# Kernel optimization log

Hardware: AMD Instinct MI355X
Metric: run time of the kernel (lower is better)

## Reference

```python
import jax, jax.numpy as jnp
import numpy as np

K = 16        # neighbors
M = 4         # repeat count
EPS = 1e-5    # BatchNorm eps (torch default)


def setup_inputs() -> dict:
    key = jax.random.key(0)
    k1, k2, k3, k4 = jax.random.split(key, 4)
    B, N, C, Fe = 8, 8192, 64, 32  # Fe = int(channels * dim_expand)
    return {
        "xyz": jax.random.normal(k1, (B, N, 3), dtype=jnp.float32),
        "feat": jax.random.normal(k2, (B, C, N), dtype=jnp.float32),
        "bn_gamma": jnp.ones((C,), jnp.float32),
        "bn_beta": jnp.zeros((C,), jnp.float32),
        "Wg": jax.random.normal(k3, (Fe, C + 3), jnp.float32) * 0.1,   # g_func weight [out, in]
        "Wh": jax.random.normal(k4, (C, M * Fe), jnp.float32) * 0.1,   # h_func weight [out, in]
    }


def reference(xyz, feat, bn_gamma, bn_beta, Wg, Wh):
    # xyz: [B, N, 3], feat: [B, C, N]
    # --- bn0: training-mode BatchNorm1d over channel dim (stats over B, N) ---
    mean = feat.mean(axis=(0, 2), keepdims=True)
    var = feat.var(axis=(0, 2), keepdims=True)
    fbn = bn_gamma[None, :, None] * (feat - mean) * jax.lax.rsqrt(var + EPS) + bn_beta[None, :, None]

    # --- g_func on concat(feat_bn, xyz^T) -> feat0 [B, N, Fe] ---
    cat = jnp.concatenate([fbn, jnp.transpose(xyz, (0, 2, 1))], axis=1)  # [B, C+3, N]
    feat0 = jnp.einsum('bcn,ec->bne', cat, Wg)                           # [B, N, Fe]

    # --- bknn: pairwise squared distances, top-k of -dist (computed once) ---
    xx = jnp.sum(xyz * xyz, axis=-1)                                     # [B, N]
    dist = xx[:, :, None] - 2.0 * jnp.einsum('bnd,bmd->bnm', xyz, xyz) + xx[:, None, :]
    _, idx = jax.lax.top_k(-dist, K)                                     # [B, N, K] int32

    # --- gather neighbor features, max-pool over K ---
    group = jax.vmap(lambda f, i: f[i])(feat0, idx)                      # [B, N, K, Fe]
    gmax = group.max(axis=2)                                             # [B, N, Fe]
    rel = gmax - feat0                                                   # [B, N, Fe]

    # Original loop reuses cached idx and feat0 every iteration, so all M
    # concatenated blocks are identical -> tile along the feature dim.
    rel_rep = jnp.concatenate([rel] * M, axis=-1)                        # [B, N, M*Fe]

    # --- h_func -> output [B, C, N] ---
    out = jnp.einsum('bnf,cf->bcn', rel_rep, Wh)
    return out
```

## Files before the change

kernel.cpp:

```cpp
#include <hip/hip_runtime.h>
#include <math.h>

#define BB 8
#define NN 8192
#define CC 64
#define FE 32
#define KN 16
#define CP3 67
#define QPW 4
#define WPB 4
#define CAPQ 64
#define YB 32
#define ZB 32
#define NCELL (YB * ZB)

__device__ double g_part[BB * CC * 2];
__device__ float g_feat0[BB * NN * FE];
__device__ int   g_idx[BB * NN * KN];
__device__ float4 g_sorted[BB * NN];
__device__ int    g_sorig[BB * NN];
__device__ unsigned g_binoff[BB * (NCELL + 1)];

__device__ __forceinline__ int cbin(float v) {
    int bi = (int)((v + 4.5f) * (32.0f / 9.0f));
    if (bi < 0) bi = 0;
    if (bi > 31) bi = 31;
    return bi;
}
__device__ __forceinline__ float frz_xx(float x, float y, float z) {
    return __fmaf_rn(z, z, __fmaf_rn(y, y, __fmul_rn(x, x)));
}

__global__ __launch_bounds__(256) void k_bnstats(const float* __restrict__ feat) {
    int bc = blockIdx.x;
    const float* p = feat + (size_t)bc * NN;
    int tid = threadIdx.x;
    double s = 0.0, s2 = 0.0;
    for (int n = tid; n < NN; n += 256) {
        double v = (double)p[n];
        s += v; s2 += v * v;
    }
    __shared__ double sh[256], sh2[256];
    sh[tid] = s; sh2[tid] = s2;
    __syncthreads();
    for (int off = 128; off > 0; off >>= 1) {
        if (tid < off) { sh[tid] += sh[tid + off]; sh2[tid] += sh2[tid + off]; }
        __syncthreads();
    }
    if (tid == 0) {
        g_part[bc * 2]     = sh[0];
        g_part[bc * 2 + 1] = sh2[0];
    }
}

__global__ __launch_bounds__(1024) void k_zbin(const float* __restrict__ xyz) {
    __shared__ unsigned hist[NCELL];
    __shared__ unsigned scan[NCELL];
    __shared__ unsigned boff[NCELL + 1];
    int b = blockIdx.x;
    int tid = threadIdx.x;
    hist[tid] = 0;
    __syncthreads();
    const float* bx = xyz + (size_t)b * NN * 3;
    for (int n = tid; n < NN; n += 1024) {
        float y = bx[n * 3 + 1], z = bx[n * 3 + 2];
        atomicAdd(&hist[cbin(y) * ZB + cbin(z)], 1u);
    }
    __syncthreads();
    scan[tid] = hist[tid];
    __syncthreads();
    for (int off = 1; off < NCELL; off <<= 1) {
        unsigned add = (tid >= off) ? scan[tid - off] : 0u;
        __syncthreads();
        scan[tid] += add;
        __syncthreads();
    }
    if (tid == 0) boff[0] = 0;
    boff[tid + 1] = scan[tid];
    __syncthreads();
    hist[tid] = 0;
    g_binoff[b * (NCELL + 1) + tid + 1] = boff[tid + 1];
    if (tid == 0) g_binoff[b * (NCELL + 1)] = 0;
    __syncthreads();
    for (int n = tid; n < NN; n += 1024) {
        const float* p = bx + (size_t)n * 3;
        float x = p[0], y = p[1], z = p[2];
        int cell = cbin(y) * ZB + cbin(z);
        unsigned pos = boff[cell] + atomicAdd(&hist[cell], 1u);
        g_sorted[(size_t)b * NN + pos] = make_float4(x, y, z, frz_xx(x, y, z));
        g_sorig[(size_t)b * NN + pos] = n;
    }
}

__global__ __launch_bounds__(256) void k_feat0(const float* __restrict__ feat,
        const float* __restrict__ xyz, const float* __restrict__ Wg,
        const float* __restrict__ gamma, const float* __restrict__ beta) {
    __shared__ float scs[CC], shs[CC];
    __shared__ float wgs[CP3 * FE];
    __shared__ float bias0[FE];
    int tid = threadIdx.x;
    if (tid < CC) {
        double s = 0.0, s2 = 0.0;
        for (int bb2 = 0; bb2 < BB; ++bb2) {
            s  += g_part[((bb2 << 6) + tid) * 2];
            s2 += g_part[((bb2 << 6) + tid) * 2 + 1];
        }
        double inv = 1.0 / (double)(BB * NN);
        double mean = s * inv;
        double var = s2 * inv - mean * mean;
        float sc = gamma[tid] * (float)(1.0 / sqrt(var + (double)1e-5f));
        scs[tid] = sc;
        shs[tid] = beta[tid] - sc * (float)mean;
    }
    __syncthreads();
    for (int i = tid; i < CP3 * FE; i += 256) {
        int c = i >> 5, e = i & 31;
        float w = Wg[e * CP3 + c];
        if (c < CC) w *= scs[c];
        wgs[c * FE + e] = w;
    }
    if (tid < FE) {
        float sacc = 0.f;
        for (int c = 0; c < CC; ++c) sacc = fmaf(Wg[tid * CP3 + c], shs[c], sacc);
        bias0[tid] = sacc;
    }
    __syncthreads();
    int b = blockIdx.x >> 5;
    int n = ((blockIdx.x & 31) << 8) + tid;
    const float* pz = xyz + ((size_t)(b * NN + n)) * 3;
    float x = pz[0], y = pz[1], z = pz[2];

    float acc[FE];
    #pragma unroll
    for (int e = 0; e < FE; ++e) acc[e] = bias0[e];
    const float* fp = feat + (size_t)b * CC * NN + n;
    for (int c = 0; c < CC; ++c) {
        float v = fp[(size_t)c * NN];
        const float4* w4 = (const float4*)(wgs + c * FE);
        #pragma unroll
        for (int e0 = 0; e0 < 8; ++e0) {
            float4 w = w4[e0];
            acc[e0 * 4 + 0] = fmaf(w.x, v, acc[e0 * 4 + 0]);
            acc[e0 * 4 + 1] = fmaf(w.y, v, acc[e0 * 4 + 1]);
            acc[e0 * 4 + 2] = fmaf(w.z, v, acc[e0 * 4 + 2]);
            acc[e0 * 4 + 3] = fmaf(w.w, v, acc[e0 * 4 + 3]);
        }
    }
    #pragma unroll
    for (int d = 0; d < 3; ++d) {
        float v = (d == 0) ? x : ((d == 1) ? y : z);
        const float4* w4 = (const float4*)(wgs + (CC + d) * FE);
        #pragma unroll
        for (int e0 = 0; e0 < 8; ++e0) {
            float4 w = w4[e0];
            acc[e0 * 4 + 0] = fmaf(w.x, v, acc[e0 * 4 + 0]);
            acc[e0 * 4 + 1] = fmaf(w.y, v, acc[e0 * 4 + 1]);
            acc[e0 * 4 + 2] = fmaf(w.z, v, acc[e0 * 4 + 2]);
            acc[e0 * 4 + 3] = fmaf(w.w, v, acc[e0 * 4 + 3]);
        }
    }
    float4* outp = (float4*)(g_feat0 + ((size_t)(b * NN + n)) * FE);
    #pragma unroll
    for (int e0 = 0; e0 < 8; ++e0)
        outp[e0] = make_float4(acc[e0 * 4 + 0], acc[e0 * 4 + 1], acc[e0 * 4 + 2], acc[e0 * 4 + 3]);
}

__global__ __launch_bounds__(256) void k_knn() {
    __shared__ unsigned long long qbuf[WPB * CAPQ];
    int tid = threadIdx.x;
    int lane = tid & 63;
    int w = tid >> 6;
    int wid = blockIdx.x * WPB + w;
    int b = wid >> 11;
    int g = wid & 2047;
    const float4* S = g_sorted + (size_t)b * NN;
    const int* SO = g_sorig + (size_t)b * NN;
    const unsigned* BO = g_binoff + b * (NCELL + 1);
    unsigned long long lt = (1ull << lane) - 1ull;
    unsigned long long* pb = qbuf + w * CAPQ;

    #pragma unroll 1
    for (int i = 0; i < QPW; ++i) {
        int qrank = g + (i << 11);
        float4 qv = S[qrank];
        float qx = qv.x, qy = qv.y, qz = qv.z, qxx = qv.w;
        int qorig = SO[qrank];
        float tt = 0.053f * __expf(qxx * (1.0f / 3.0f));
        float t0 = tt > 3.f ? 3.f : tt;
        float tlo = 0.f, thi = 0.f;
        unsigned cnt = 0;

        for (int attempt = 0; attempt < 40; ++attempt) {
            cnt = 0;
            float tpe = t0 + 1e-3f;
            float R = __fsqrt_rn(tpe) + 1e-3f;
            int ylo = cbin(qy - R), yhi = cbin(qy + R);

            int yb = ylo, p = 0, hi = 0;
            {
                float rowlo = 0.28125f * (float)yb - 4.5f;
                float dy = fmaxf(0.f, fmaxf(rowlo - qy, qy - (rowlo + 0.28125f)));
                float rz2 = tpe - dy * dy;
                if (rz2 > 0.f) {
                    float Rz = __fsqrt_rn(rz2) + 1e-3f;
                    int zl = cbin(qz - Rz), zh = cbin(qz + Rz);
                    p = (int)BO[yb * ZB + zl]; hi = (int)BO[yb * ZB + zh + 1];
                }
            }
            while (p >= hi && yb < yhi) {
                ++yb;
                float rowlo = 0.28125f * (float)yb - 4.5f;
                float dy = fmaxf(0.f, fmaxf(rowlo - qy, qy - (rowlo + 0.28125f)));
                float rz2 = tpe - dy * dy;
                if (rz2 > 0.f) {
                    float Rz = __fsqrt_rn(rz2) + 1e-3f;
                    int zl = cbin(qz - Rz), zh = cbin(qz + Rz);
                    p = (int)BO[yb * ZB + zl]; hi = (int)BO[yb * ZB + zh + 1];
                } else { p = 0; hi = 0; }
            }
            bool have = p < hi;
            int jc0 = 0, jc1 = 0; bool in0 = false, in1 = false;
            float4 c0, c1;
            if (have) {
                int base = p + 2 * lane;
                jc0 = base < hi ? base : hi - 1;
                jc1 = base + 1 < hi ? base + 1 : hi - 1;
                c0 = S[jc0]; c1 = S[jc1];
                in0 = base < hi; in1 = base + 1 < hi;
            }
            while (have) {
                int yb2 = yb, p2 = p + 128, hi2 = hi;
                while (p2 >= hi2 && yb2 < yhi) {
                    ++yb2;
                    float rowlo = 0.28125f * (float)yb2 - 4.5f;
                    float dy = fmaxf(0.f, fmaxf(rowlo - qy, qy - (rowlo + 0.28125f)));
                    float rz2 = tpe - dy * dy;
                    if (rz2 > 0.f) {
                        float Rz = __fsqrt_rn(rz2) + 1e-3f;
                        int zl = cbin(qz - Rz), zh = cbin(qz + Rz);
                        p2 = (int)BO[yb2 * ZB + zl]; hi2 = (int)BO[yb2 * ZB + zh + 1];
                    } else { p2 = 0; hi2 = 0; }
                }
                bool have2 = p2 < hi2;
                int jn0 = jc0, jn1 = jc1; bool inn0 = false, inn1 = false;
                float4 n0 = c0, n1 = c1;
                if (have2) {
                    int base = p2 + 2 * lane;
                    jn0 = base < hi2 ? base : hi2 - 1;
                    jn1 = base + 1 < hi2 ? base + 1 : hi2 - 1;
                    n0 = S[jn0]; n1 = S[jn1];
                    inn0 = base < hi2; inn1 = base + 1 < hi2;
                }
                float dot0 = __fmaf_rn(qz, c0.z, __fmaf_rn(qy, c0.y, __fmul_rn(qx, c0.x)));
                float dist0 = __fadd_rn(__fmaf_rn(-2.f, dot0, qxx), c0.w);
                float dot1 = __fmaf_rn(qz, c1.z, __fmaf_rn(qy, c1.y, __fmul_rn(qx, c1.x)));
                float dist1 = __fadd_rn(__fmaf_rn(-2.f, dot1, qxx), c1.w);
                bool pr0 = (dist0 <= t0) && in0;
                bool pr1 = (dist1 <= t0) && in1;
                unsigned long long m0 = __ballot(pr0);
                unsigned long long m1 = __ballot(pr1);
                if (m0 | m1) {
                    unsigned n0c = (unsigned)__popcll(m0);
                    unsigned pos0 = cnt + (unsigned)__popcll(m0 & lt);
                    unsigned pos1 = cnt + n0c + (unsigned)__popcll(m1 & lt);
                    if (pr0 && pos0 < CAPQ) {
                        int corig = SO[jc0];
                        int db = __float_as_int(dist0);
                        unsigned key = (unsigned)db ^ (unsigned)((db >> 31) | 0x80000000);
                        pb[pos0] = ((unsigned long long)key << 32) | (unsigned)corig;
                    }
                    if (pr1 && pos1 < CAPQ) {
                        int corig = SO[jc1];
                        int db = __float_as_int(dist1);
                        unsigned key = (unsigned)db ^ (unsigned)((db >> 31) | 0x80000000);
                        pb[pos1] = ((unsigned long long)key << 32) | (unsigned)corig;
                    }
                    cnt += n0c + (unsigned)__popcll(m1);
                }
                yb = yb2; p = p2; hi = hi2; have = have2;
                jc0 = jn0; jc1 = jn1; c0 = n0; c1 = n1; in0 = inn0; in1 = inn1;
            }
            if (cnt < KN) {
                tlo = t0;
                t0 = (thi > 0.f) ? __fsqrt_rn(tlo * thi) : t0 * 2.0f;
            } else if (cnt > CAPQ) {
                thi = t0;
                t0 = (tlo > 0.f) ? __fsqrt_rn(tlo * thi) : t0 * 0.5f;
            } else break;
        }

        unsigned tot = cnt > CAPQ ? CAPQ : cnt;
        unsigned long long e0 = ((unsigned)lane < tot) ? pb[lane] : ~0ull;
        unsigned rank0 = 0;
        for (unsigned jx = 0; jx < tot; ++jx) {
            unsigned long long v = pb[jx];
            rank0 += (v < e0) ? 1u : 0u;
        }
        if (((unsigned)lane < tot) && rank0 < KN)
            g_idx[(b * NN + qorig) * KN + rank0] = (int)(e0 & 0xffffffffull);
    }
}

__global__ __launch_bounds__(256) void k_out(const float* __restrict__ Wh,
        float* __restrict__ out) {
    __shared__ float whs[CC * FE];
    int tid = threadIdx.x;
    for (int i = tid; i < CC * FE; i += 256) {
        int c = i >> 5, e = i & 31;
        float s = 0.f;
        #pragma unroll
        for (int m = 0; m < 4; ++m) s += Wh[c * 128 + m * 32 + e];
        whs[i] = s;
    }
    __syncthreads();
    int b = blockIdx.x >> 5;
    int n = ((blockIdx.x & 31) << 8) + tid;
    const int* ip = g_idx + (size_t)(b * NN + n) * KN;
    const float4* f0 = (const float4*)(g_feat0 + (size_t)b * NN * FE);
    float gmax[FE];
    #pragma unroll
    for (int e = 0; e < FE; ++e) gmax[e] = -__builtin_inff();
    for (int k = 0; k < KN; ++k) {
        int id = ip[k] & (NN - 1);
        const float4* row = f0 + (size_t)id * 8;
        #pragma unroll
        for (int e0 = 0; e0 < 8; ++e0) {
            float4 v = row[e0];
            gmax[e0 * 4 + 0] = fmaxf(gmax[e0 * 4 + 0], v.x);
            gmax[e0 * 4 + 1] = fmaxf(gmax[e0 * 4 + 1], v.y);
            gmax[e0 * 4 + 2] = fmaxf(gmax[e0 * 4 + 2], v.z);
            gmax[e0 * 4 + 3] = fmaxf(gmax[e0 * 4 + 3], v.w);
        }
    }
    const float4* selfr = f0 + (size_t)n * 8;
    float rel[FE];
    #pragma unroll
    for (int e0 = 0; e0 < 8; ++e0) {
        float4 v = selfr[e0];
        rel[e0 * 4 + 0] = gmax[e0 * 4 + 0] - v.x;
        rel[e0 * 4 + 1] = gmax[e0 * 4 + 1] - v.y;
        rel[e0 * 4 + 2] = gmax[e0 * 4 + 2] - v.z;
        rel[e0 * 4 + 3] = gmax[e0 * 4 + 3] - v.w;
    }
    float* op = out + (size_t)b * CC * NN + n;
    for (int c = 0; c < CC; ++c) {
        const float4* w4 = (const float4*)(whs + c * FE);
        float s = 0.f;
        #pragma unroll
        for (int e0 = 0; e0 < 8; ++e0) {
            float4 w = w4[e0];
            s = fmaf(w.x, rel[e0 * 4 + 0], s);
            s = fmaf(w.y, rel[e0 * 4 + 1], s);
            s = fmaf(w.z, rel[e0 * 4 + 2], s);
            s = fmaf(w.w, rel[e0 * 4 + 3], s);
        }
        op[(size_t)c * NN] = s;
    }
}

extern "C" void kernel_launch(void* const* d_in, const int* in_sizes, int n_in,
                              void* d_out, int out_size, void* d_ws, size_t ws_size,
                              hipStream_t stream) {
    const float* xyz   = (const float*)d_in[0];
    const float* feat  = (const float*)d_in[1];
    const float* gamma = (const float*)d_in[2];
    const float* beta  = (const float*)d_in[3];
    const float* Wg    = (const float*)d_in[4];
    const float* Wh    = (const float*)d_in[5];
    float* out = (float*)d_out;
    (void)d_ws; (void)ws_size;

    hipLaunchKernelGGL(k_bnstats, dim3(512),  dim3(256),  0, stream, feat);
    hipLaunchKernelGGL(k_zbin,    dim3(8),    dim3(1024), 0, stream, xyz);
    hipLaunchKernelGGL(k_feat0,   dim3(256),  dim3(256),  0, stream, feat, xyz, Wg, gamma, beta);
    hipLaunchKernelGGL(k_knn,     dim3(4096), dim3(256),  0, stream);
    hipLaunchKernelGGL(k_out,     dim3(256),  dim3(256),  0, stream, Wh, out);
}
```

Before: 201.0 us.

## Split per-point work across multiple threads in feat0 and output kernels

k_feat0 now gives each point to two threads, each computing 16 of the 32 features, and launches twice as many blocks. k_out gives each point to four threads: each gathers 4 of the 16 neighbors, the partial maxima are combined through shared memory, and each thread then computes 16 of the 64 output channels. This raises parallelism and occupancy in two kernels that previously launched only 256 blocks on a large GPU. The cost is a shared-memory reduction, a block barrier, and less coalesced feat loads and output stores, since adjacent threads now share a point.

```diff
diff --git a/kernel.cpp b/kernel.cpp
--- a/kernel.cpp
+++ b/kernel.cpp
@@ -125,20 +125,22 @@
         bias0[tid] = sacc;
     }
     __syncthreads();
-    int b = blockIdx.x >> 5;
-    int n = ((blockIdx.x & 31) << 8) + tid;
+    int pid = blockIdx.x * 128 + (tid >> 1);
+    int half = tid & 1;
+    int b = pid >> 13;
+    int n = pid & (NN - 1);
     const float* pz = xyz + ((size_t)(b * NN + n)) * 3;
     float x = pz[0], y = pz[1], z = pz[2];
 
-    float acc[FE];
-    #pragma unroll
-    for (int e = 0; e < FE; ++e) acc[e] = bias0[e];
+    float acc[16];
+    #pragma unroll
+    for (int e = 0; e < 16; ++e) acc[e] = bias0[half * 16 + e];
     const float* fp = feat + (size_t)b * CC * NN + n;
     for (int c = 0; c < CC; ++c) {
         float v = fp[(size_t)c * NN];
-        const float4* w4 = (const float4*)(wgs + c * FE);
-        #pragma unroll
-        for (int e0 = 0; e0 < 8; ++e0) {
+        const float4* w4 = (const float4*)(wgs + c * FE) + half * 4;
+        #pragma unroll
+        for (int e0 = 0; e0 < 4; ++e0) {
             float4 w = w4[e0];
             acc[e0 * 4 + 0] = fmaf(w.x, v, acc[e0 * 4 + 0]);
             acc[e0 * 4 + 1] = fmaf(w.y, v, acc[e0 * 4 + 1]);
@@ -149,9 +151,9 @@
     #pragma unroll
     for (int d = 0; d < 3; ++d) {
         float v = (d == 0) ? x : ((d == 1) ? y : z);
-        const float4* w4 = (const float4*)(wgs + (CC + d) * FE);
-        #pragma unroll
-        for (int e0 = 0; e0 < 8; ++e0) {
+        const float4* w4 = (const float4*)(wgs + (CC + d) * FE) + half * 4;
+        #pragma unroll
+        for (int e0 = 0; e0 < 4; ++e0) {
             float4 w = w4[e0];
             acc[e0 * 4 + 0] = fmaf(w.x, v, acc[e0 * 4 + 0]);
             acc[e0 * 4 + 1] = fmaf(w.y, v, acc[e0 * 4 + 1]);
@@ -159,9 +161,9 @@
             acc[e0 * 4 + 3] = fmaf(w.w, v, acc[e0 * 4 + 3]);
         }
     }
-    float4* outp = (float4*)(g_feat0 + ((size_t)(b * NN + n)) * FE);
-    #pragma unroll
-    for (int e0 = 0; e0 < 8; ++e0)
+    float4* outp = ((float4*)(g_feat0 + ((size_t)(b * NN + n)) * FE)) + half * 4;
+    #pragma unroll
+    for (int e0 = 0; e0 < 4; ++e0)
         outp[e0] = make_float4(acc[e0 * 4 + 0], acc[e0 * 4 + 1], acc[e0 * 4 + 2], acc[e0 * 4 + 3]);
 }
 
@@ -304,6 +306,7 @@
 __global__ __launch_bounds__(256) void k_out(const float* __restrict__ Wh,
         float* __restrict__ out) {
     __shared__ float whs[CC * FE];
+    __shared__ float pmax[64][4][33];
     int tid = threadIdx.x;
     for (int i = tid; i < CC * FE; i += 256) {
         int c = i >> 5, e = i & 31;
@@ -312,38 +315,48 @@
         for (int m = 0; m < 4; ++m) s += Wh[c * 128 + m * 32 + e];
         whs[i] = s;
     }
-    __syncthreads();
-    int b = blockIdx.x >> 5;
-    int n = ((blockIdx.x & 31) << 8) + tid;
-    const int* ip = g_idx + (size_t)(b * NN + n) * KN;
+    int pt = tid >> 2, part = tid & 3;
+    int pid = blockIdx.x * 64 + pt;
+    int b = pid >> 13;
+    int n = pid & (NN - 1);
+    const int* ip = g_idx + (size_t)(b * NN + n) * KN + part * 4;
     const float4* f0 = (const float4*)(g_feat0 + (size_t)b * NN * FE);
-    float gmax[FE];
-    #pragma unroll
-    for (int e = 0; e < FE; ++e) gmax[e] = -__builtin_inff();
-    for (int k = 0; k < KN; ++k) {
+    float gm[FE];
+    #pragma unroll
+    for (int e = 0; e < FE; ++e) gm[e] = -__builtin_inff();
+    #pragma unroll
+    for (int k = 0; k < 4; ++k) {
         int id = ip[k] & (NN - 1);
         const float4* row = f0 + (size_t)id * 8;
         #pragma unroll
         for (int e0 = 0; e0 < 8; ++e0) {
             float4 v = row[e0];
-            gmax[e0 * 4 + 0] = fmaxf(gmax[e0 * 4 + 0], v.x);
-            gmax[e0 * 4 + 1] = fmaxf(gmax[e0 * 4 + 1], v.y);
-            gmax[e0 * 4 + 2] = fmaxf(gmax[e0 * 4 + 2], v.z);
-            gmax[e0 * 4 + 3] = fmaxf(gmax[e0 * 4 + 3], v.w);
-        }
-    }
+            gm[e0 * 4 + 0] = fmaxf(gm[e0 * 4 + 0], v.x);
+            gm[e0 * 4 + 1] = fmaxf(gm[e0 * 4 + 1], v.y);
+            gm[e0 * 4 + 2] = fmaxf(gm[e0 * 4 + 2], v.z);
+            gm[e0 * 4 + 3] = fmaxf(gm[e0 * 4 + 3], v.w);
+        }
+    }
+    #pragma unroll
+    for (int e = 0; e < FE; ++e) pmax[pt][part][e] = gm[e];
+    __syncthreads();
+
     const float4* selfr = f0 + (size_t)n * 8;
     float rel[FE];
     #pragma unroll
     for (int e0 = 0; e0 < 8; ++e0) {
         float4 v = selfr[e0];
-        rel[e0 * 4 + 0] = gmax[e0 * 4 + 0] - v.x;
-        rel[e0 * 4 + 1] = gmax[e0 * 4 + 1] - v.y;
-        rel[e0 * 4 + 2] = gmax[e0 * 4 + 2] - v.z;
-        rel[e0 * 4 + 3] = gmax[e0 * 4 + 3] - v.w;
+        #pragma unroll
+        for (int j = 0; j < 4; ++j) {
+            int e = e0 * 4 + j;
+            float gg = fmaxf(fmaxf(pmax[pt][0][e], pmax[pt][1][e]),
+                             fmaxf(pmax[pt][2][e], pmax[pt][3][e]));
+            float sv = (j == 0) ? v.x : (j == 1) ? v.y : (j == 2) ? v.z : v.w;
+            rel[e] = gg - sv;
+        }
     }
     float* op = out + (size_t)b * CC * NN + n;
-    for (int c = 0; c < CC; ++c) {
+    for (int c = part * 16; c < part * 16 + 16; ++c) {
         const float4* w4 = (const float4*)(whs + c * FE);
         float s = 0.f;
         #pragma unroll
@@ -372,7 +385,7 @@
 
     hipLaunchKernelGGL(k_bnstats, dim3(512),  dim3(256),  0, stream, feat);
     hipLaunchKernelGGL(k_zbin,    dim3(8),    dim3(1024), 0, stream, xyz);
-    hipLaunchKernelGGL(k_feat0,   dim3(256),  dim3(256),  0, stream, feat, xyz, Wg, gamma, beta);
+    hipLaunchKernelGGL(k_feat0,   dim3(512),  dim3(256),  0, stream, feat, xyz, Wg, gamma, beta);
     hipLaunchKernelGGL(k_knn,     dim3(4096), dim3(256),  0, stream);
-    hipLaunchKernelGGL(k_out,     dim3(256),  dim3(256),  0, stream, Wh, out);
-}
+    hipLaunchKernelGGL(k_out,     dim3(1024), dim3(256),  0, stream, Wh, out);
+}
```

After: 190.4 us. -5.3%, faster.
